# Kernel optimization log

Measured on AMD Instinct MI355X. Metric: run time of the kernel, lower is better.

The kernel has to match this reference:

```python
import jax, jax.numpy as jnp
import numpy as np

B = 131072      # batch
D = 768         # input_dim (RoBERTa hidden)
P = 8           # num_primary_caps
PD = 16         # primary_cap_dim
C = 5           # num_class_caps
CD = 16         # class_cap_dim
ITERS = 3       # num_routing_iterations


def squash(s, axis=-1):
    # squash(s) = (|s|^2 / (1+|s|^2)) * s / (|s| + 1e-8)
    sq = jnp.sum(s * s, axis=axis, keepdims=True)
    return (sq / (1.0 + sq)) * s / (jnp.sqrt(sq) + 1e-8)


def setup_inputs() -> dict:
    key = jax.random.key(0)
    k1, k2, k3, k4 = jax.random.split(key, 4)
    x = jax.random.normal(k1, (B, D), dtype=jnp.float32)
    lim = 1.0 / np.sqrt(D)  # torch nn.Linear default init range
    Wp = jax.random.uniform(k2, (P, D, PD), jnp.float32, -lim, lim)   # stacked 8 Linear weights (in->out)
    bp = jax.random.uniform(k3, (P, PD), jnp.float32, -lim, lim)      # stacked biases
    xav = np.sqrt(2.0 / (PD + CD))
    W = jax.random.normal(k4, (P, C, PD, CD), dtype=jnp.float32) * xav  # routing transform
    return {"x": x, "Wp": Wp, "bp": bp, "W": W}


def reference(x, Wp, bp, W):
    # primary capsules: 8 separate Linear(768,16) + squash, batched as one einsum
    u = squash(jnp.einsum('bi,pio->bpo', x, Wp) + bp)          # [B, P, PD]
    # votes u_hat[b,p,c,:] = u[b,p,:] @ W[p,c,:,:]
    u_hat = jnp.einsum('bpi,pcij->bpcj', u, W)                 # [B, P, C, CD]
    b = jnp.zeros((x.shape[0], P, C), dtype=x.dtype)
    v = None
    for it in range(ITERS):
        c = jax.nn.softmax(b, axis=2)                          # [B, P, C]
        s = jnp.sum(c[..., None] * u_hat, axis=1)              # [B, C, CD]
        v = squash(s, axis=-1)                                 # [B, C, CD]
        if it < ITERS - 1:
            agreement = jnp.sum(u_hat * v[:, None], axis=-1)   # [B, P, C]
            b = b + agreement
    return v
```

## Files before the change

kernel.cpp:

```cpp
#include <hip/hip_runtime.h>
#include <math.h>


#define BATCH 131072
#define DDIM  768
#define NC    5
#define NPD   16
#define BM    64
#define NKS   24

typedef __attribute__((ext_vector_type(8))) short short8;
typedef __attribute__((ext_vector_type(4))) float f32x4;

#define WLDS(p,c,i) ((((p)*NC+(c))*NPD+(i))*16 + (p)*4)
#define UA_OFF    10272
#define UA_STRIDE 136
#define SMEM_FLOATS (UA_OFF + 16*UA_STRIDE)

__device__ __forceinline__ unsigned short f2b_rne(float f) {
    unsigned u = __builtin_bit_cast(unsigned, f);
    u += 0x7fffu + ((u >> 16) & 1u);
    return (unsigned short)(u >> 16);
}
__device__ __forceinline__ float b2f(unsigned short h) {
    unsigned u = ((unsigned)h) << 16;
    return __builtin_bit_cast(float, u);
}
template<int CTRL>
__device__ __forceinline__ float dpp_add(float v) {
    int s = __builtin_amdgcn_update_dpp(0, __builtin_bit_cast(int, v),
                                        CTRL, 0xf, 0xf, false);
    return v + __builtin_bit_cast(float, s);
}
__device__ __forceinline__ float rowsum16(float v) {
    v = dpp_add<0x121>(v); v = dpp_add<0x122>(v);
    v = dpp_add<0x124>(v); v = dpp_add<0x128>(v);
    return v;
}
__device__ __forceinline__ float rowsum8(float v) {
    v = dpp_add<0x122>(v); v = dpp_add<0x124>(v); v = dpp_add<0x128>(v);
    return v;
}
__device__ __forceinline__ float pairsum(float v) { return dpp_add<0xB1>(v); }

__global__ void caps_prep_wp(const float* __restrict__ Wp,
                             unsigned short* __restrict__ wpt) {
    const int idx = blockIdx.x * 256 + threadIdx.x;
    const int ks  = idx >> 12;
    const int r   = idx & 4095;
    const int col = r >> 5;
    const int k   = r & 31;
    wpt[ks * 4096 + col * 32 + k] =
        f2b_rne(Wp[(col >> 4) * (DDIM * NPD) + (ks * 32 + k) * NPD + (col & 15)]);
}

__global__ __launch_bounds__(256, 3)
void caps_main(const float* __restrict__ x, const float* __restrict__ bp,
               const float* __restrict__ Wg,
               const unsigned short* __restrict__ wpt,
               float* __restrict__ out)
{
    __shared__ float smf[SMEM_FLOATS];
    char* smc = (char*)smf;
    const int tid  = threadIdx.x;
    const int w    = tid >> 6;
    const int lane = tid & 63;
    const int ln   = lane & 15;
    const int g    = lane >> 4;
    const int b0   = blockIdx.x * BM;

    f32x4 acc[8];
#pragma unroll
    for (int t = 0; t < 8; ++t) acc[t] = (f32x4){0.f, 0.f, 0.f, 0.f};

    const float* xrow = x + (size_t)(b0 + w * 16 + ln) * DDIM + g * 8;
    const char*  wptc = (const char*)wpt;

    f32x4 sa = *(const f32x4*)(wptc + tid * 32);
    f32x4 sb = *(const f32x4*)(wptc + tid * 32 + 16);
    f32x4 xa = __builtin_nontemporal_load((const f32x4*)xrow);
    f32x4 xb = __builtin_nontemporal_load((const f32x4*)(xrow + 4));
    *(f32x4*)(smc + tid * 32)      = sa;
    *(f32x4*)(smc + tid * 32 + 16) = sb;
    __syncthreads();

    for (int ks = 0; ks < NKS; ++ks) {
        const char* cur = smc + (ks & 1) * 8192;
        char*       nxt = smc + ((ks + 1) & 1) * 8192;
        f32x4 nxa, nxb;
        if (ks < NKS - 1) {
            const char* wim = wptc + (size_t)(ks + 1) * 8192;
            sa = *(const f32x4*)(wim + tid * 32);
            sb = *(const f32x4*)(wim + tid * 32 + 16);
            nxa = __builtin_nontemporal_load((const f32x4*)(xrow + (ks + 1) * 32));
            nxb = __builtin_nontemporal_load((const f32x4*)(xrow + (ks + 1) * 32 + 4));
        }
        const float av[8] = {xa[0], xa[1], xa[2], xa[3], xb[0], xb[1], xb[2], xb[3]};
        short8 ah, al;
#pragma unroll
        for (int e = 0; e < 8; ++e) {
            const unsigned short h = f2b_rne(av[e]);
            ah[e] = (short)h;
            al[e] = (short)f2b_rne(av[e] - b2f(h));
        }
#pragma unroll
        for (int t = 0; t < 8; ++t) {
            const short8 bh = *(const short8*)(cur + (t * 16 + ln) * 64 + g * 16);
            acc[t] = __builtin_amdgcn_mfma_f32_16x16x32_bf16(ah, bh, acc[t], 0, 0, 0);
            acc[t] = __builtin_amdgcn_mfma_f32_16x16x32_bf16(al, bh, acc[t], 0, 0, 0);
        }
        if (ks < NKS - 1) {
            *(f32x4*)(nxt + tid * 32)      = sa;
            *(f32x4*)(nxt + tid * 32 + 16) = sb;
            xa = nxa; xb = nxb;
        }
        __syncthreads();
    }

    {
        const f32x4* wg4 = (const f32x4*)Wg;
#pragma unroll
        for (int q = 0; q < 10; ++q) {
            const int f4i  = q * 256 + tid;
            const int flat = f4i * 4;
            const int p    = flat / 1280;
            f32x4 wv = wg4[f4i];
            *(f32x4*)&smf[flat + p * 4] = wv;
        }
    }

    const int tm = tid >> 4, tn = tid & 15;
    const int pp = tn >> 1, jh = tn & 1, j0 = jh * 8;
    float bb[16];
#pragma unroll
    for (int q = 0; q < 4; ++q) {
        f32x4 b4 = *(const f32x4*)(bp + pp * NPD + q * 4);
        bb[q * 4 + 0] = b4[0]; bb[q * 4 + 1] = b4[1];
        bb[q * 4 + 2] = b4[2]; bb[q * 4 + 3] = b4[3];
    }
    float* uA = smf + UA_OFF;

    for (int p = 0; p < 4; ++p) {
#pragma unroll
        for (int pc = 0; pc < 4; ++pc) if (pc == p) {
#pragma unroll
            for (int t = 0; t < 8; ++t)
                uA[(w * 4 + g) * UA_STRIDE + t * 16 + ln] = acc[t][pc];
        }
        __syncthreads();

        float u[16];
#pragma unroll
        for (int q = 0; q < 4; ++q) {
            f32x4 u4 = *(const f32x4*)&uA[tm * UA_STRIDE + pp * NPD + q * 4];
            u[q * 4 + 0] = u4[0] + bb[q * 4 + 0];
            u[q * 4 + 1] = u4[1] + bb[q * 4 + 1];
            u[q * 4 + 2] = u4[2] + bb[q * 4 + 2];
            u[q * 4 + 3] = u4[3] + bb[q * 4 + 3];
        }
        float sq = 0.f;
#pragma unroll
        for (int q = 0; q < 16; ++q) sq = fmaf(u[q], u[q], sq);
        const float scl = (sq / (1.f + sq)) * (1.f / (sqrtf(sq) + 1e-8f));
#pragma unroll
        for (int q = 0; q < 16; ++q) u[q] *= scl;

        float uh[NC][8];
#pragma unroll
        for (int c = 0; c < NC; ++c) {
#pragma unroll
            for (int jj = 0; jj < 8; ++jj) uh[c][jj] = 0.f;
#pragma unroll
            for (int q = 0; q < 16; ++q) {
                const float* wr = &smf[WLDS(pp, c, q) + j0];
                f32x4 w0 = *(const f32x4*)(wr);
                f32x4 w1 = *(const f32x4*)(wr + 4);
                const float uq = u[q];
                uh[c][0] = fmaf(uq, w0[0], uh[c][0]);
                uh[c][1] = fmaf(uq, w0[1], uh[c][1]);
                uh[c][2] = fmaf(uq, w0[2], uh[c][2]);
                uh[c][3] = fmaf(uq, w0[3], uh[c][3]);
                uh[c][4] = fmaf(uq, w1[0], uh[c][4]);
                uh[c][5] = fmaf(uq, w1[1], uh[c][5]);
                uh[c][6] = fmaf(uq, w1[2], uh[c][6]);
                uh[c][7] = fmaf(uq, w1[3], uh[c][7]);
            }
        }

        float blog[NC] = {0.f, 0.f, 0.f, 0.f, 0.f};
        float s[NC][8];
#pragma unroll
        for (int itr = 0; itr < 3; ++itr) {
            float m = blog[0];
#pragma unroll
            for (int c = 1; c < NC; ++c) m = fmaxf(m, blog[c]);
            float e[NC]; float es = 0.f;
#pragma unroll
            for (int c = 0; c < NC; ++c) { e[c] = __expf(blog[c] - m); es += e[c]; }
            const float inv = 1.f / es;
#pragma unroll
            for (int c = 0; c < NC; ++c) {
                const float cc = e[c] * inv;
#pragma unroll
                for (int jj = 0; jj < 8; ++jj) s[c][jj] = cc * uh[c][jj];
            }
#pragma unroll
            for (int c = 0; c < NC; ++c)
#pragma unroll
                for (int jj = 0; jj < 8; ++jj) s[c][jj] = rowsum8(s[c][jj]);
#pragma unroll
            for (int c = 0; c < NC; ++c) {
                float ss = 0.f;
#pragma unroll
                for (int jj = 0; jj < 8; ++jj) ss = fmaf(s[c][jj], s[c][jj], ss);
                ss = pairsum(ss);
                const float vs = (ss / (1.f + ss)) * (1.f / (sqrtf(ss) + 1e-8f));
#pragma unroll
                for (int jj = 0; jj < 8; ++jj) s[c][jj] *= vs;
            }
            if (itr < 2) {
#pragma unroll
                for (int c = 0; c < NC; ++c) {
                    float a = 0.f;
#pragma unroll
                    for (int jj = 0; jj < 8; ++jj) a = fmaf(uh[c][jj], s[c][jj], a);
                    a = pairsum(a);
                    blog[c] += a;
                }
            }
        }

        if (pp < NC) {
            float o[8];
#pragma unroll
            for (int jj = 0; jj < 8; ++jj) o[jj] = s[0][jj];
#pragma unroll
            for (int c = 1; c < NC; ++c) {
                const bool sel = (pp == c);
#pragma unroll
                for (int jj = 0; jj < 8; ++jj) o[jj] = sel ? s[c][jj] : o[jj];
            }
            const int row_glob = b0 + (tm >> 2) * 16 + (tm & 3) * 4 + p;
            float* og = out + (size_t)row_glob * (NC * NPD) + pp * NPD + j0;
            const f32x4 o0 = {o[0], o[1], o[2], o[3]};
            const f32x4 o1 = {o[4], o[5], o[6], o[7]};
            __builtin_nontemporal_store(o0, (f32x4*)og);
            __builtin_nontemporal_store(o1, (f32x4*)(og + 4));
        }
        if (p < 3) __syncthreads();
    }
}

extern "C" void kernel_launch(void* const* d_in, const int* in_sizes, int n_in,
                              void* d_out, int out_size, void* d_ws, size_t ws_size,
                              hipStream_t stream) {
    (void)in_sizes; (void)n_in; (void)ws_size; (void)out_size;
    const float* x  = (const float*)d_in[0];
    const float* Wp = (const float*)d_in[1];
    const float* bp = (const float*)d_in[2];
    const float* W  = (const float*)d_in[3];
    float* out = (float*)d_out;
    unsigned short* wpt = (unsigned short*)d_ws;

    caps_prep_wp<<<384, 256, 0, stream>>>(Wp, wpt);
    caps_main<<<BATCH / BM, 256, 0, stream>>>(x, bp, W, wpt, out);
}
```

Before: 284.7 us.

## Split fused kernel into GEMM and routing kernels via workspace buffer

Breaks the single fused kernel into a bf16-split MFMA GEMM kernel that writes primary-capsule pre-activations to workspace, and a separate routing kernel that reads them back, processes two rows per thread and computes votes and dynamic routing. The batch is processed in chunks sized to the available workspace. This removes the serial per-row LDS staging and barriers in the fused epilogue and lets each kernel pick its own occupancy. In exchange it adds a global write and read of the intermediate (512 bytes per row) and may need several launches if the workspace is small.

```diff
diff --git a/kernel.cpp b/kernel.cpp
--- a/kernel.cpp
+++ b/kernel.cpp
@@ -1,4 +1,5 @@
 #include <hip/hip_runtime.h>
+#include <hip/hip_bf16.h>
 #include <math.h>
 
 
@@ -12,10 +13,8 @@
 typedef __attribute__((ext_vector_type(8))) short short8;
 typedef __attribute__((ext_vector_type(4))) float f32x4;
 
+#define WS_UPRE_OFF 196608
 #define WLDS(p,c,i) ((((p)*NC+(c))*NPD+(i))*16 + (p)*4)
-#define UA_OFF    10272
-#define UA_STRIDE 136
-#define SMEM_FLOATS (UA_OFF + 16*UA_STRIDE)
 
 __device__ __forceinline__ unsigned short f2b_rne(float f) {
     unsigned u = __builtin_bit_cast(unsigned, f);
@@ -31,11 +30,6 @@
     int s = __builtin_amdgcn_update_dpp(0, __builtin_bit_cast(int, v),
                                         CTRL, 0xf, 0xf, false);
     return v + __builtin_bit_cast(float, s);
-}
-__device__ __forceinline__ float rowsum16(float v) {
-    v = dpp_add<0x121>(v); v = dpp_add<0x122>(v);
-    v = dpp_add<0x124>(v); v = dpp_add<0x128>(v);
-    return v;
 }
 __device__ __forceinline__ float rowsum8(float v) {
     v = dpp_add<0x122>(v); v = dpp_add<0x124>(v); v = dpp_add<0x128>(v);
@@ -55,25 +49,23 @@
 }
 
 __global__ __launch_bounds__(256, 3)
-void caps_main(const float* __restrict__ x, const float* __restrict__ bp,
-               const float* __restrict__ Wg,
+void caps_gemm(const float* __restrict__ x,
                const unsigned short* __restrict__ wpt,
-               float* __restrict__ out)
+               float* __restrict__ upre, int row0)
 {
-    __shared__ float smf[SMEM_FLOATS];
-    char* smc = (char*)smf;
+    __shared__ char smc[16384];
     const int tid  = threadIdx.x;
     const int w    = tid >> 6;
     const int lane = tid & 63;
     const int ln   = lane & 15;
     const int g    = lane >> 4;
-    const int b0   = blockIdx.x * BM;
+    const int brel = blockIdx.x * BM;
 
     f32x4 acc[8];
 #pragma unroll
     for (int t = 0; t < 8; ++t) acc[t] = (f32x4){0.f, 0.f, 0.f, 0.f};
 
-    const float* xrow = x + (size_t)(b0 + w * 16 + ln) * DDIM + g * 8;
+    const float* xrow = x + (size_t)(row0 + brel + w * 16 + ln) * DDIM + g * 8;
     const char*  wptc = (const char*)wpt;
 
     f32x4 sa = *(const f32x4*)(wptc + tid * 32);
@@ -99,9 +91,11 @@
         short8 ah, al;
 #pragma unroll
         for (int e = 0; e < 8; ++e) {
-            const unsigned short h = f2b_rne(av[e]);
+            const unsigned short h =
+                __builtin_bit_cast(unsigned short, __float2bfloat16(av[e]));
             ah[e] = (short)h;
-            al[e] = (short)f2b_rne(av[e] - b2f(h));
+            al[e] = (short)__builtin_bit_cast(unsigned short,
+                        __float2bfloat16(av[e] - b2f(h)));
         }
 #pragma unroll
         for (int t = 0; t < 8; ++t) {
@@ -117,6 +111,20 @@
         __syncthreads();
     }
 
+    const int rbase = brel + w * 16 + g * 4;
+#pragma unroll
+    for (int t = 0; t < 8; ++t)
+#pragma unroll
+        for (int r = 0; r < 4; ++r)
+            upre[(size_t)(rbase + r) * 128 + t * 16 + ln] = acc[t][r];
+}
+
+__global__ __launch_bounds__(256, 2)
+void caps_route(const float* __restrict__ upre, const float* __restrict__ bp,
+                const float* __restrict__ Wg, float* __restrict__ out, int row0)
+{
+    __shared__ float smf[10272];
+    const int tid = threadIdx.x;
     {
         const f32x4* wg4 = (const f32x4*)Wg;
 #pragma unroll
@@ -128,9 +136,12 @@
             *(f32x4*)&smf[flat + p * 4] = wv;
         }
     }
-
-    const int tm = tid >> 4, tn = tid & 15;
+    __syncthreads();
+
+    const int pg = tid >> 4, tn = tid & 15;
     const int pp = tn >> 1, jh = tn & 1, j0 = jh * 8;
+    const int rrel = blockIdx.x * 32 + pg * 2;
+
     float bb[16];
 #pragma unroll
     for (int q = 0; q < 4; ++q) {
@@ -138,55 +149,58 @@
         bb[q * 4 + 0] = b4[0]; bb[q * 4 + 1] = b4[1];
         bb[q * 4 + 2] = b4[2]; bb[q * 4 + 3] = b4[3];
     }
-    float* uA = smf + UA_OFF;
-
-    for (int p = 0; p < 4; ++p) {
-#pragma unroll
-        for (int pc = 0; pc < 4; ++pc) if (pc == p) {
-#pragma unroll
-            for (int t = 0; t < 8; ++t)
-                uA[(w * 4 + g) * UA_STRIDE + t * 16 + ln] = acc[t][pc];
-        }
-        __syncthreads();
-
-        float u[16];
+
+    float u[2][16];
+#pragma unroll
+    for (int r = 0; r < 2; ++r) {
+        const float* ur = upre + (size_t)(rrel + r) * 128 + pp * NPD;
 #pragma unroll
         for (int q = 0; q < 4; ++q) {
-            f32x4 u4 = *(const f32x4*)&uA[tm * UA_STRIDE + pp * NPD + q * 4];
-            u[q * 4 + 0] = u4[0] + bb[q * 4 + 0];
-            u[q * 4 + 1] = u4[1] + bb[q * 4 + 1];
-            u[q * 4 + 2] = u4[2] + bb[q * 4 + 2];
-            u[q * 4 + 3] = u4[3] + bb[q * 4 + 3];
+            f32x4 u4 = *(const f32x4*)(ur + q * 4);
+            u[r][q * 4 + 0] = u4[0] + bb[q * 4 + 0];
+            u[r][q * 4 + 1] = u4[1] + bb[q * 4 + 1];
+            u[r][q * 4 + 2] = u4[2] + bb[q * 4 + 2];
+            u[r][q * 4 + 3] = u4[3] + bb[q * 4 + 3];
         }
         float sq = 0.f;
 #pragma unroll
-        for (int q = 0; q < 16; ++q) sq = fmaf(u[q], u[q], sq);
+        for (int q = 0; q < 16; ++q) sq = fmaf(u[r][q], u[r][q], sq);
         const float scl = (sq / (1.f + sq)) * (1.f / (sqrtf(sq) + 1e-8f));
 #pragma unroll
-        for (int q = 0; q < 16; ++q) u[q] *= scl;
-
-        float uh[NC][8];
-#pragma unroll
-        for (int c = 0; c < NC; ++c) {
-#pragma unroll
-            for (int jj = 0; jj < 8; ++jj) uh[c][jj] = 0.f;
-#pragma unroll
-            for (int q = 0; q < 16; ++q) {
-                const float* wr = &smf[WLDS(pp, c, q) + j0];
-                f32x4 w0 = *(const f32x4*)(wr);
-                f32x4 w1 = *(const f32x4*)(wr + 4);
-                const float uq = u[q];
-                uh[c][0] = fmaf(uq, w0[0], uh[c][0]);
-                uh[c][1] = fmaf(uq, w0[1], uh[c][1]);
-                uh[c][2] = fmaf(uq, w0[2], uh[c][2]);
-                uh[c][3] = fmaf(uq, w0[3], uh[c][3]);
-                uh[c][4] = fmaf(uq, w1[0], uh[c][4]);
-                uh[c][5] = fmaf(uq, w1[1], uh[c][5]);
-                uh[c][6] = fmaf(uq, w1[2], uh[c][6]);
-                uh[c][7] = fmaf(uq, w1[3], uh[c][7]);
-            }
-        }
-
+        for (int q = 0; q < 16; ++q) u[r][q] *= scl;
+    }
+
+    float uh[2][NC][8];
+#pragma unroll
+    for (int r = 0; r < 2; ++r)
+#pragma unroll
+        for (int c = 0; c < NC; ++c)
+#pragma unroll
+            for (int jj = 0; jj < 8; ++jj) uh[r][c][jj] = 0.f;
+#pragma unroll
+    for (int c = 0; c < NC; ++c) {
+#pragma unroll
+        for (int q = 0; q < 16; ++q) {
+            const float* wr = &smf[WLDS(pp, c, q) + j0];
+            f32x4 w0 = *(const f32x4*)(wr);
+            f32x4 w1 = *(const f32x4*)(wr + 4);
+#pragma unroll
+            for (int r = 0; r < 2; ++r) {
+                const float uq = u[r][q];
+                uh[r][c][0] = fmaf(uq, w0[0], uh[r][c][0]);
+                uh[r][c][1] = fmaf(uq, w0[1], uh[r][c][1]);
+                uh[r][c][2] = fmaf(uq, w0[2], uh[r][c][2]);
+                uh[r][c][3] = fmaf(uq, w0[3], uh[r][c][3]);
+                uh[r][c][4] = fmaf(uq, w1[0], uh[r][c][4]);
+                uh[r][c][5] = fmaf(uq, w1[1], uh[r][c][5]);
+                uh[r][c][6] = fmaf(uq, w1[2], uh[r][c][6]);
+                uh[r][c][7] = fmaf(uq, w1[3], uh[r][c][7]);
+            }
+        }
+    }
+
+#pragma unroll
+    for (int r = 0; r < 2; ++r) {
         float blog[NC] = {0.f, 0.f, 0.f, 0.f, 0.f};
         float s[NC][8];
 #pragma unroll
@@ -202,7 +216,7 @@
             for (int c = 0; c < NC; ++c) {
                 const float cc = e[c] * inv;
 #pragma unroll
-                for (int jj = 0; jj < 8; ++jj) s[c][jj] = cc * uh[c][jj];
+                for (int jj = 0; jj < 8; ++jj) s[c][jj] = cc * uh[r][c][jj];
             }
 #pragma unroll
             for (int c = 0; c < NC; ++c)
@@ -223,7 +237,7 @@
                 for (int c = 0; c < NC; ++c) {
                     float a = 0.f;
 #pragma unroll
-                    for (int jj = 0; jj < 8; ++jj) a = fmaf(uh[c][jj], s[c][jj], a);
+                    for (int jj = 0; jj < 8; ++jj) a = fmaf(uh[r][c][jj], s[c][jj], a);
                     a = pairsum(a);
                     blog[c] += a;
                 }
@@ -240,28 +254,36 @@
 #pragma unroll
                 for (int jj = 0; jj < 8; ++jj) o[jj] = sel ? s[c][jj] : o[jj];
             }
-            const int row_glob = b0 + (tm >> 2) * 16 + (tm & 3) * 4 + p;
-            float* og = out + (size_t)row_glob * (NC * NPD) + pp * NPD + j0;
-            const f32x4 o0 = {o[0], o[1], o[2], o[3]};
-            const f32x4 o1 = {o[4], o[5], o[6], o[7]};
-            __builtin_nontemporal_store(o0, (f32x4*)og);
-            __builtin_nontemporal_store(o1, (f32x4*)(og + 4));
-        }
-        if (p < 3) __syncthreads();
+            float* og = out + (size_t)(row0 + rrel + r) * (NC * NPD) + pp * NPD + j0;
+            *(f32x4*)(og)     = (f32x4){o[0], o[1], o[2], o[3]};
+            *(f32x4*)(og + 4) = (f32x4){o[4], o[5], o[6], o[7]};
+        }
     }
 }
 
 extern "C" void kernel_launch(void* const* d_in, const int* in_sizes, int n_in,
                               void* d_out, int out_size, void* d_ws, size_t ws_size,
                               hipStream_t stream) {
-    (void)in_sizes; (void)n_in; (void)ws_size; (void)out_size;
+    (void)in_sizes; (void)n_in; (void)out_size;
     const float* x  = (const float*)d_in[0];
     const float* Wp = (const float*)d_in[1];
     const float* bp = (const float*)d_in[2];
     const float* W  = (const float*)d_in[3];
     float* out = (float*)d_out;
+
     unsigned short* wpt = (unsigned short*)d_ws;
+    float* upre = (float*)((char*)d_ws + WS_UPRE_OFF);
 
     caps_prep_wp<<<384, 256, 0, stream>>>(Wp, wpt);
-    caps_main<<<BATCH / BM, 256, 0, stream>>>(x, bp, W, wpt, out);
-}
+
+    long chunk = 0;
+    if (ws_size > WS_UPRE_OFF)
+        chunk = (long)((ws_size - WS_UPRE_OFF) / 512) / 64 * 64;
+    if (chunk <= 0) chunk = 64;
+    if (chunk > BATCH) chunk = BATCH;
+    for (long r0 = 0; r0 < BATCH; r0 += chunk) {
+        long n = BATCH - r0; if (n > chunk) n = chunk;
+        caps_gemm <<<(int)(n / 64), 256, 0, stream>>>(x, wpt, upre, (int)r0);
+        caps_route<<<(int)(n / 32), 256, 0, stream>>>(upre, bp, W, out, (int)r0);
+    }
+}
```

After: 1.124 ms. 3.95x slower.
